# Kernel optimization log

Measured on AMD Instinct MI355X. Metric: run time of the kernel, lower is better.

Reference implementation:

```python
import jax, jax.numpy as jnp
import numpy as np
import math

B, N, DMODEL, H = 8, 1024, 256, 8
HEAD_DIM = DMODEL // H


def setup_inputs() -> dict:
    key = jax.random.key(0)
    ks = jax.random.split(key, 8)
    x = jax.random.normal(ks[0], (B, N, DMODEL), dtype=jnp.float32)
    # symmetric-ish nonnegative pairwise distances
    adj = jax.random.uniform(ks[1], (B, N, N), dtype=jnp.float32) * 10.0
    mask = jax.random.uniform(ks[2], (B, N)) < 0.9  # bool, mostly valid nodes
    W_qkv = jax.random.normal(ks[3], (DMODEL, 3 * DMODEL), dtype=jnp.float32) / math.sqrt(DMODEL)
    b_qkv = jax.random.normal(ks[4], (3 * DMODEL,), dtype=jnp.float32) * 0.01
    shifts = jnp.arange(1.0, H + 1.0, dtype=jnp.float32)  # initial_shifts
    widths = jnp.ones((H,), dtype=jnp.float32)            # initial_widths
    # self_loop_W = 1/head_dim + U(0,1), non-trainable
    self_loop_w = 1.0 / HEAD_DIM + jax.random.uniform(ks[5], (H,), dtype=jnp.float32)
    return {"x": x, "adj": adj, "mask": mask, "W_qkv": W_qkv, "b_qkv": b_qkv,
            "shifts": shifts, "widths": widths, "self_loop_w": self_loop_w}


def reference(x, adj, mask, W_qkv, b_qkv, shifts, widths, self_loop_w):
    b, n, _ = x.shape
    h = shifts.shape[0]
    d = W_qkv.shape[1] // (3 * h)
    qkv = (x @ W_qkv + b_qkv).reshape(b, n, 3, h, d)
    qkv = jnp.transpose(qkv, (2, 0, 3, 1, 4))  # [3, B, H, N, D]
    Q, K, V = qkv[0], qkv[1], qkv[2]
    scores = jnp.einsum('bhnd,bhmd->bhnm', Q, K) / jnp.sqrt(jnp.float32(d))
    # Gaussian moire focus on adjacency distances, per head
    sh = shifts.reshape(1, h, 1, 1)
    w = jnp.maximum(widths, 0.5).reshape(1, h, 1, 1)
    moire = jnp.exp(-((adj[:, None, :, :] - sh) ** 2) / w)
    adjusted = scores + jnp.log(jnp.maximum(moire, 1e-6))
    eye = jnp.eye(n, dtype=adjusted.dtype)  # [N, N]
    adjusted = adjusted + eye * self_loop_w.reshape(1, h, 1, 1)
    mask2d = (mask[:, :, None] & mask[:, None, :])[:, None, :, :]  # [B,1,N,N]
    adjusted = jnp.where(mask2d, adjusted, jnp.float32(-1000000.0))
    attn = jax.nn.softmax(adjusted, axis=-1)
    out = jnp.einsum('bhnm,bhmd->bhnd', attn, V)
    return jnp.transpose(out, (0, 2, 1, 3)).reshape(b, n, h * d)
```

## Files before the change

### kernel.cpp

```cpp
#include <hip/hip_runtime.h>

#define BB 8
#define NN 1024
#define DM 256
#define HH 8
#define HD 32
#define TC 768

typedef __bf16 bf16x8 __attribute__((ext_vector_type(8)));
typedef __bf16 bf16x4 __attribute__((ext_vector_type(4)));
typedef float  f32x4  __attribute__((ext_vector_type(4)));

__global__ __launch_bounds__(256) void precast(
    const float* __restrict__ x, const float* __restrict__ W,
    __bf16* __restrict__ xb, __bf16* __restrict__ Wt)
{
  const int tid = threadIdx.x;
  const int bid = blockIdx.x;
  if (bid < 48) {
    __shared__ __bf16 T[64][65];
    const int ct = bid % 12, kt = bid / 12;
    const int c0 = ct * 64, k0 = kt * 64;
    #pragma unroll
    for (int i = 0; i < 16; ++i) {
      int e = tid + i * 256, kk = e >> 6, cc = e & 63;
      T[cc][kk] = (__bf16)W[(size_t)(k0 + kk) * TC + c0 + cc];
    }
    __syncthreads();
    #pragma unroll
    for (int i = 0; i < 16; ++i) {
      int e = tid + i * 256, cc = e >> 6, kk = e & 63;
      Wt[(size_t)(c0 + cc) * DM + k0 + kk] = T[cc][kk];
    }
  } else {
    const size_t e = (size_t)(bid - 48) * 256 + tid;
    const float4 v = ((const float4*)x)[e];
    bf16x4 o;
    o[0] = (__bf16)v.x; o[1] = (__bf16)v.y;
    o[2] = (__bf16)v.z; o[3] = (__bf16)v.w;
    ((bf16x4*)xb)[e] = o;
  }
}

__global__ __launch_bounds__(256, 4) void qkv_gemm(
    const __bf16* __restrict__ xb, const __bf16* __restrict__ Wt,
    const float* __restrict__ bias, __bf16* __restrict__ Qb,
    __bf16* __restrict__ Kb, __bf16* __restrict__ Vt)
{
  __shared__ __align__(16) char U[18432];
  __bf16* As = (__bf16*)U;
  __bf16* Bs = (__bf16*)(U + 10240);

  const int tid  = threadIdx.x;
  const int w    = tid >> 6, lane = tid & 63;
  const int n16  = lane & 15, quad = lane >> 4;
  const int m0   = blockIdx.y * 128, c0 = blockIdx.x * 64;
  const int bb   = m0 >> 10, n0 = m0 & 1023;

  const int arow = tid >> 1, ahalf = tid & 1;
  const int bc   = tid & 63, bkh = tid >> 6;

  f32x4 acc[2][4] = {};

  const __bf16* xa_base = &xb[(size_t)(m0 + arow) * DM + ahalf * 16];
  const __bf16* wb_base = &Wt[(size_t)(c0 + bc) * DM + bkh * 8];
  bf16x8 ra0 = *(const bf16x8*)&xa_base[0];
  bf16x8 ra1 = *(const bf16x8*)&xa_base[8];
  bf16x8 rb  = *(const bf16x8*)&wb_base[0];

  for (int k0 = 0; k0 < DM; k0 += 32) {
    *(bf16x8*)&As[arow*40 + ahalf*16]     = ra0;
    *(bf16x8*)&As[arow*40 + ahalf*16 + 8] = ra1;
    *(bf16x8*)&Bs[bc*40 + bkh*8]          = rb;
    __syncthreads();
    if (k0 + 32 < DM) {
      ra0 = *(const bf16x8*)&xa_base[k0 + 32];
      ra1 = *(const bf16x8*)&xa_base[k0 + 40];
      rb  = *(const bf16x8*)&wb_base[k0 + 32];
    }
    bf16x8 af0 = *(const bf16x8*)&As[(w*32 + n16)*40 + quad*8];
    bf16x8 af1 = *(const bf16x8*)&As[(w*32 + 16 + n16)*40 + quad*8];
    #pragma unroll
    for (int cb = 0; cb < 4; ++cb) {
      bf16x8 bf = *(const bf16x8*)&Bs[(cb*16 + n16)*40 + quad*8];
      acc[0][cb] = __builtin_amdgcn_mfma_f32_16x16x32_bf16(af0, bf, acc[0][cb], 0, 0, 0);
      acc[1][cb] = __builtin_amdgcn_mfma_f32_16x16x32_bf16(af1, bf, acc[1][cb], 0, 0, 0);
    }
    __syncthreads();
  }

  float bv[4];
  #pragma unroll
  for (int cb = 0; cb < 4; ++cb) bv[cb] = bias[c0 + cb*16 + n16];

  if (c0 < 512) {
    __bf16* Ct = (__bf16*)U;
    #pragma unroll
    for (int cb = 0; cb < 4; ++cb)
      #pragma unroll
      for (int mb = 0; mb < 2; ++mb)
        #pragma unroll
        for (int r = 0; r < 4; ++r)
          Ct[(w*32 + mb*16 + quad*4 + r)*72 + cb*16 + n16] =
              (__bf16)(acc[mb][cb][r] + bv[cb]);
    __syncthreads();
    const int chunk = tid & 3, hh = (tid >> 2) & 1, rbase = tid >> 3;
    const int c_head = c0 + hh*32;
    const int h = (c_head >> 5) & 7;
    __bf16* base = (c_head >> 8) ? Kb : Qb;
    #pragma unroll
    for (int it = 0; it < 4; ++it) {
      int rl = rbase + it*32;
      bf16x8 v = *(const bf16x8*)&Ct[rl*72 + hh*32 + chunk*8];
      *(bf16x8*)&base[((size_t)((bb*HH + h)*NN + n0 + rl))*HD + chunk*8] = v;
    }
  } else {
    __bf16* CtT = (__bf16*)U;
    #pragma unroll
    for (int cb = 0; cb < 4; ++cb)
      #pragma unroll
      for (int mb = 0; mb < 2; ++mb) {
        bf16x4 t;
        #pragma unroll
        for (int r = 0; r < 4; ++r) t[r] = (__bf16)(acc[mb][cb][r] + bv[cb]);
        *(bf16x4*)&CtT[(cb*16 + n16)*136 + w*32 + mb*16 + quad*4] = t;
      }
    __syncthreads();
    const int col = tid >> 2, sg = tid & 3;
    const int c = c0 + col;
    const int h = (c >> 5) & 7, dd = c & 31;
    __bf16* dst = &Vt[((size_t)((bb*HH + h)*HD + dd))*NN + n0 + sg*32];
    const __bf16* srcp = &CtT[col*136 + sg*32];
    #pragma unroll
    for (int q2 = 0; q2 < 4; ++q2)
      *(bf16x8*)&dst[q2*8] = *(const bf16x8*)&srcp[q2*8];
  }
}

__global__ __launch_bounds__(256, 4) void attn_kernel(
    const __bf16* __restrict__ Q, const __bf16* __restrict__ K,
    const __bf16* __restrict__ Vt, const float* __restrict__ adj,
    const int* __restrict__ mask, const float* __restrict__ shifts,
    const float* __restrict__ widths, const float* __restrict__ slw,
    float* __restrict__ out)
{
  __shared__ __align__(16) char U[9216];
  __bf16 (*Qs)[40] = (__bf16(*)[40])U;
  __bf16 (*Ps)[72] = (__bf16(*)[72])U;
  __shared__ __align__(16) __bf16 Ks[2][64][40];
  __shared__ __align__(16) __bf16 Vts[2][32][72];

  const int tid  = threadIdx.x;
  const int w    = tid >> 6, lane = tid & 63;
  const int n16  = lane & 15, quad = lane >> 4;
  const int bh   = blockIdx.x >> 4, qt = blockIdx.x & 15;
  const int b    = bh >> 3, h = bh & 7;
  const int q0   = qt * 64;

  const float L2E   = 1.4426950408889634f;
  const float sh    = shifts[h];
  const float ninvw = -L2E / fmaxf(widths[h], 0.5f);
  const float slv   = slw[h] * L2E;
  const float scl   = 0.17677669529663687f * L2E;
  const float MASKV = -28.0f;
  const float c1 = -2.0f * sh * ninvw;
  const float c2 = sh * sh * ninvw;

  const int srow = tid >> 2, sseg = tid & 3;
  const int vd   = tid >> 3, vsg  = tid & 7;

  {
    const __bf16* Qg = Q + (size_t)(bh*NN + q0)*HD;
    *(bf16x8*)&Qs[srow][sseg*8] = *(const bf16x8*)&Qg[srow*HD + sseg*8];
  }
  const __bf16* Kg = K + (size_t)bh*NN*HD;
  const __bf16* Vg = Vt + (size_t)bh*HD*NN;
  {
    *(bf16x8*)&Ks[0][srow][sseg*8] = *(const bf16x8*)&Kg[srow*HD + sseg*8];
    *(bf16x8*)&Vts[0][vd][vsg*8]   = *(const bf16x8*)&Vg[(size_t)vd*NN + vsg*8];
  }
  int mq[4];
  #pragma unroll
  for (int r = 0; r < 4; ++r) mq[r] = mask[b*NN + q0 + w*16 + quad*4 + r];
  __syncthreads();
  const bf16x8 qf = *(const bf16x8*)&Qs[w*16 + n16][quad*8];
  __syncthreads();

  const f32x4 zero = {0.f, 0.f, 0.f, 0.f};
  float l_r[4] = {0.f, 0.f, 0.f, 0.f};
  f32x4 o0 = zero, o1 = zero;

  const float* arow0 = adj + ((size_t)(b*NN + q0 + w*16 + quad*4))*NN + n16;
  const float* arow1 = arow0 + NN;
  const float* arow2 = arow0 + 2*NN;
  const float* arow3 = arow0 + 3*NN;
  const int*   mrp   = mask + b*NN + n16;

  #pragma unroll 2
  for (int jtl = 0; jtl < 16; ++jtl) {
    const int cur = jtl & 1;
    const int j0  = jtl * 64;

    bf16x8 kn, vn;
    if (jtl < 15) {
      kn = *(const bf16x8*)&Kg[(j0 + 64 + srow)*HD + sseg*8];
      vn = *(const bf16x8*)&Vg[(size_t)vd*NN + j0 + 64 + vsg*8];
    }

    int mj[4];
    #pragma unroll
    for (int cb = 0; cb < 4; ++cb) mj[cb] = mrp[cb*16];
    float av[4][4];
    #pragma unroll
    for (int cb = 0; cb < 4; ++cb) {
      av[0][cb] = arow0[cb*16];
      av[1][cb] = arow1[cb*16];
      av[2][cb] = arow2[cb*16];
      av[3][cb] = arow3[cb*16];
    }

    f32x4 s[4];
    #pragma unroll
    for (int cb = 0; cb < 4; ++cb) {
      bf16x8 kf = *(const bf16x8*)&Ks[cur][cb*16 + n16][quad*8];
      s[cb] = __builtin_amdgcn_mfma_f32_16x16x32_bf16(qf, kf, zero, 0, 0, 0);
    }

    const bool diagtile = (jtl == qt);
    #pragma unroll
    for (int r = 0; r < 4; ++r) {
      const int rowl = w*16 + quad*4 + r;
      #pragma unroll
      for (int cb = 0; cb < 4; ++cb) {
        float a   = av[r][cb];
        float mo  = fmaf(a, fmaf(a, ninvw, c1), c2);
        float val = fmaf(s[cb][r], scl, mo);
        if (diagtile && (cb*16 + n16 == rowl)) val += slv;
        bool ok = (mq[r] != 0) && (mj[cb] != 0);
        val = ok ? val : MASKV;
        float p = __builtin_amdgcn_exp2f(val);
        l_r[r] += p;
        Ps[rowl][cb*16 + n16] = (__bf16)p;
      }
    }

    bf16x8 a0  = *(const bf16x8*)&Ps[w*16 + n16][quad*8];
    bf16x8 a1  = *(const bf16x8*)&Ps[w*16 + n16][32 + quad*8];
    bf16x8 b00 = *(const bf16x8*)&Vts[cur][n16][quad*8];
    bf16x8 b01 = *(const bf16x8*)&Vts[cur][n16][32 + quad*8];
    bf16x8 b10 = *(const bf16x8*)&Vts[cur][16 + n16][quad*8];
    bf16x8 b11 = *(const bf16x8*)&Vts[cur][16 + n16][32 + quad*8];
    o0 = __builtin_amdgcn_mfma_f32_16x16x32_bf16(a0, b00, o0, 0, 0, 0);
    o0 = __builtin_amdgcn_mfma_f32_16x16x32_bf16(a1, b01, o0, 0, 0, 0);
    o1 = __builtin_amdgcn_mfma_f32_16x16x32_bf16(a0, b10, o1, 0, 0, 0);
    o1 = __builtin_amdgcn_mfma_f32_16x16x32_bf16(a1, b11, o1, 0, 0, 0);

    if (jtl < 15) {
      *(bf16x8*)&Ks[1 - cur][srow][sseg*8] = kn;
      *(bf16x8*)&Vts[1 - cur][vd][vsg*8]   = vn;
    }
    arow0 += 64; arow1 += 64; arow2 += 64; arow3 += 64; mrp += 64;
    __syncthreads();
  }

  #pragma unroll
  for (int r = 0; r < 4; ++r) {
    float l = l_r[r];
    l += __shfl_xor(l, 1); l += __shfl_xor(l, 2);
    l += __shfl_xor(l, 4); l += __shfl_xor(l, 8);
    const float invl = 1.0f / l;
    const int n = q0 + w*16 + quad*4 + r;
    float* og = out + ((size_t)(b*NN + n))*DM + h*HD;
    og[n16]      = o0[r] * invl;
    og[16 + n16] = o1[r] * invl;
  }
}

extern "C" void kernel_launch(void* const* d_in, const int* in_sizes, int n_in,
                              void* d_out, int out_size, void* d_ws, size_t ws_size,
                              hipStream_t stream) {
  const float* x      = (const float*)d_in[0];
  const float* adj    = (const float*)d_in[1];
  const int*   mask   = (const int*)d_in[2];
  const float* W      = (const float*)d_in[3];
  const float* bias   = (const float*)d_in[4];
  const float* shifts = (const float*)d_in[5];
  const float* widths = (const float*)d_in[6];
  const float* slwp   = (const float*)d_in[7];
  float* out = (float*)d_out;

  const size_t BHND = (size_t)BB*HH*NN*HD;
  const size_t WTN  = (size_t)TC*DM;
  __bf16* xbuf = (__bf16*)d_ws;
  __bf16* Wt   = xbuf + BHND;
  __bf16* Qb   = Wt + WTN;
  __bf16* Kb   = Qb + BHND;
  __bf16* Vt   = Kb + BHND;

  precast<<<dim3(48 + (int)(BHND/4/256)), 256, 0, stream>>>(x, W, xbuf, Wt);
  qkv_gemm<<<dim3(TC/64, (BB*NN)/128), 256, 0, stream>>>(xbuf, Wt, bias, Qb, Kb, Vt);
  attn_kernel<<<dim3(BB*HH*16), 256, 0, stream>>>(Qb, Kb, Vt, adj, mask,
                                                  shifts, widths, slwp, out);
}
```

Before: 134.8 us.

## Prefetch adj tile one step ahead, swizzle P in LDS, compute row sums via MFMA

Result: slower. 140.3 us (+4.1%).

```diff
diff --git a/kernel.cpp b/kernel.cpp
--- a/kernel.cpp
+++ b/kernel.cpp
@@ -145,7 +145,6 @@
     float* __restrict__ out)
 {
   __shared__ __align__(16) char U[9216];
-  __bf16 (*Qs)[40] = (__bf16(*)[40])U;
   __bf16 (*Ps)[72] = (__bf16(*)[72])U;
   __shared__ __align__(16) __bf16 Ks[2][64][40];
   __shared__ __align__(16) __bf16 Vts[2][32][72];
@@ -169,12 +168,12 @@
   const int srow = tid >> 2, sseg = tid & 3;
   const int vd   = tid >> 3, vsg  = tid & 7;
 
-  {
-    const __bf16* Qg = Q + (size_t)(bh*NN + q0)*HD;
-    *(bf16x8*)&Qs[srow][sseg*8] = *(const bf16x8*)&Qg[srow*HD + sseg*8];
-  }
   const __bf16* Kg = K + (size_t)bh*NN*HD;
   const __bf16* Vg = Vt + (size_t)bh*HD*NN;
+
+  const bf16x8 qf =
+      *(const bf16x8*)&Q[((size_t)bh*NN + q0 + w*16 + n16)*HD + quad*8];
+
   {
     *(bf16x8*)&Ks[0][srow][sseg*8] = *(const bf16x8*)&Kg[srow*HD + sseg*8];
     *(bf16x8*)&Vts[0][vd][vsg*8]   = *(const bf16x8*)&Vg[(size_t)vd*NN + vsg*8];
@@ -182,13 +181,6 @@
   int mq[4];
   #pragma unroll
   for (int r = 0; r < 4; ++r) mq[r] = mask[b*NN + q0 + w*16 + quad*4 + r];
-  __syncthreads();
-  const bf16x8 qf = *(const bf16x8*)&Qs[w*16 + n16][quad*8];
-  __syncthreads();
-
-  const f32x4 zero = {0.f, 0.f, 0.f, 0.f};
-  float l_r[4] = {0.f, 0.f, 0.f, 0.f};
-  f32x4 o0 = zero, o1 = zero;
 
   const float* arow0 = adj + ((size_t)(b*NN + q0 + w*16 + quad*4))*NN + n16;
   const float* arow1 = arow0 + NN;
@@ -196,27 +188,48 @@
   const float* arow3 = arow0 + 3*NN;
   const int*   mrp   = mask + b*NN + n16;
 
+  float av[2][4][4];
+  int   mj[2][4];
+  #pragma unroll
+  for (int cb = 0; cb < 4; ++cb) mj[0][cb] = mrp[cb*16];
+  #pragma unroll
+  for (int cb = 0; cb < 4; ++cb) {
+    av[0][0][cb] = arow0[cb*16];
+    av[0][1][cb] = arow1[cb*16];
+    av[0][2][cb] = arow2[cb*16];
+    av[0][3][cb] = arow3[cb*16];
+  }
+  arow0 += 64; arow1 += 64; arow2 += 64; arow3 += 64; mrp += 64;
+
+  const f32x4 zero = {0.f, 0.f, 0.f, 0.f};
+  f32x4 o0 = zero, o1 = zero, lacc = zero;
+  bf16x8 onesb;
+  #pragma unroll
+  for (int i = 0; i < 8; ++i) onesb[i] = (__bf16)1.0f;
+
+  const int sa = (n16 & 12) << 1;
+
+  __syncthreads();
+
   #pragma unroll 2
   for (int jtl = 0; jtl < 16; ++jtl) {
-    const int cur = jtl & 1;
+    const int cur = jtl & 1, nxt = cur ^ 1;
     const int j0  = jtl * 64;
 
     bf16x8 kn, vn;
     if (jtl < 15) {
       kn = *(const bf16x8*)&Kg[(j0 + 64 + srow)*HD + sseg*8];
       vn = *(const bf16x8*)&Vg[(size_t)vd*NN + j0 + 64 + vsg*8];
-    }
-
-    int mj[4];
-    #pragma unroll
-    for (int cb = 0; cb < 4; ++cb) mj[cb] = mrp[cb*16];
-    float av[4][4];
-    #pragma unroll
-    for (int cb = 0; cb < 4; ++cb) {
-      av[0][cb] = arow0[cb*16];
-      av[1][cb] = arow1[cb*16];
-      av[2][cb] = arow2[cb*16];
-      av[3][cb] = arow3[cb*16];
+      #pragma unroll
+      for (int cb = 0; cb < 4; ++cb) mj[nxt][cb] = mrp[cb*16];
+      #pragma unroll
+      for (int cb = 0; cb < 4; ++cb) {
+        av[nxt][0][cb] = arow0[cb*16];
+        av[nxt][1][cb] = arow1[cb*16];
+        av[nxt][2][cb] = arow2[cb*16];
+        av[nxt][3][cb] = arow3[cb*16];
+      }
+      arow0 += 64; arow1 += 64; arow2 += 64; arow3 += 64; mrp += 64;
     }
 
     f32x4 s[4];
@@ -232,43 +245,40 @@
       const int rowl = w*16 + quad*4 + r;
       #pragma unroll
       for (int cb = 0; cb < 4; ++cb) {
-        float a   = av[r][cb];
+        float a   = av[cur][r][cb];
         float mo  = fmaf(a, fmaf(a, ninvw, c1), c2);
         float val = fmaf(s[cb][r], scl, mo);
         if (diagtile && (cb*16 + n16 == rowl)) val += slv;
-        bool ok = (mq[r] != 0) && (mj[cb] != 0);
+        bool ok = (mq[r] != 0) && (mj[cur][cb] != 0);
         val = ok ? val : MASKV;
         float p = __builtin_amdgcn_exp2f(val);
-        l_r[r] += p;
-        Ps[rowl][cb*16 + n16] = (__bf16)p;
+        Ps[rowl][(cb*16 + n16) ^ (quad*8)] = (__bf16)p;
       }
     }
 
-    bf16x8 a0  = *(const bf16x8*)&Ps[w*16 + n16][quad*8];
-    bf16x8 a1  = *(const bf16x8*)&Ps[w*16 + n16][32 + quad*8];
+    bf16x8 a0  = *(const bf16x8*)&Ps[w*16 + n16][(quad*8) ^ sa];
+    bf16x8 a1  = *(const bf16x8*)&Ps[w*16 + n16][32 + ((quad*8) ^ sa)];
     bf16x8 b00 = *(const bf16x8*)&Vts[cur][n16][quad*8];
     bf16x8 b01 = *(const bf16x8*)&Vts[cur][n16][32 + quad*8];
     bf16x8 b10 = *(const bf16x8*)&Vts[cur][16 + n16][quad*8];
     bf16x8 b11 = *(const bf16x8*)&Vts[cur][16 + n16][32 + quad*8];
-    o0 = __builtin_amdgcn_mfma_f32_16x16x32_bf16(a0, b00, o0, 0, 0, 0);
-    o0 = __builtin_amdgcn_mfma_f32_16x16x32_bf16(a1, b01, o0, 0, 0, 0);
-    o1 = __builtin_amdgcn_mfma_f32_16x16x32_bf16(a0, b10, o1, 0, 0, 0);
-    o1 = __builtin_amdgcn_mfma_f32_16x16x32_bf16(a1, b11, o1, 0, 0, 0);
+    o0   = __builtin_amdgcn_mfma_f32_16x16x32_bf16(a0, b00, o0, 0, 0, 0);
+    o0   = __builtin_amdgcn_mfma_f32_16x16x32_bf16(a1, b01, o0, 0, 0, 0);
+    o1   = __builtin_amdgcn_mfma_f32_16x16x32_bf16(a0, b10, o1, 0, 0, 0);
+    o1   = __builtin_amdgcn_mfma_f32_16x16x32_bf16(a1, b11, o1, 0, 0, 0);
+    lacc = __builtin_amdgcn_mfma_f32_16x16x32_bf16(a0, onesb, lacc, 0, 0, 0);
+    lacc = __builtin_amdgcn_mfma_f32_16x16x32_bf16(a1, onesb, lacc, 0, 0, 0);
 
     if (jtl < 15) {
-      *(bf16x8*)&Ks[1 - cur][srow][sseg*8] = kn;
-      *(bf16x8*)&Vts[1 - cur][vd][vsg*8]   = vn;
-    }
-    arow0 += 64; arow1 += 64; arow2 += 64; arow3 += 64; mrp += 64;
+      *(bf16x8*)&Ks[nxt][srow][sseg*8] = kn;
+      *(bf16x8*)&Vts[nxt][vd][vsg*8]   = vn;
+    }
     __syncthreads();
   }
 
   #pragma unroll
   for (int r = 0; r < 4; ++r) {
-    float l = l_r[r];
-    l += __shfl_xor(l, 1); l += __shfl_xor(l, 2);
-    l += __shfl_xor(l, 4); l += __shfl_xor(l, 8);
-    const float invl = 1.0f / l;
+    const float invl = 1.0f / lacc[r];
     const int n = q0 + w*16 + quad*4 + r;
     float* og = out + ((size_t)(b*NN + n))*DM + h*HD;
     og[n16]      = o0[r] * invl;
```
